# Kernel optimization log

Measured on AMD Instinct MI355X. Metric: run time of the kernel, lower is better.

The kernel has to match this reference:

```python
import jax, jax.numpy as jnp
import numpy as np

N_NODES = 20000
HEADS = 4


def _gat_conv(x, src, dst, W, att_src, att_dst, bias, concat):
    # PyG GATConv: h = x @ W -> [N, H, C]; edge score = leaky_relu(a_s[src]+a_d[dst], 0.2);
    # segment softmax over dst; scatter-add weighted messages.
    N = x.shape[0]
    H, C = att_src.shape[1], att_src.shape[2]
    h = (x @ W).reshape(N, H, C)
    a_s = jnp.sum(h * att_src, axis=-1)  # [N, H]
    a_d = jnp.sum(h * att_dst, axis=-1)  # [N, H]
    e = jax.nn.leaky_relu(a_s[src] + a_d[dst], negative_slope=0.2)  # [E, H]
    m = jax.ops.segment_max(e, dst, num_segments=N)  # [N, H]
    e = jnp.exp(e - m[dst])
    denom = jax.ops.segment_sum(e, dst, num_segments=N)
    alpha = e / (denom[dst] + 1e-16)  # [E, H]
    msg = h[src] * alpha[:, :, None]  # [E, H, C]
    out = jax.ops.segment_sum(msg, dst, num_segments=N)  # [N, H, C]
    if concat:
        out = out.reshape(N, H * C)
    else:
        out = out.mean(axis=1)
    return out + bias


def setup_inputs() -> dict:
    key = jax.random.key(0)
    ks = jax.random.split(key, 16)
    N, F_in, Hd, H, Z = N_NODES, 256, 128, HEADS, 64
    E = 320000
    x = jax.random.normal(ks[0], (N, F_in), dtype=jnp.float32)
    edge_index = jax.random.randint(ks[1], (2, E), 0, N, dtype=jnp.int64)
    def xavier(k, shape):
        fan_in, fan_out = shape[0], shape[1]
        lim = float(np.sqrt(6.0 / (fan_in + fan_out)))
        return jax.random.uniform(k, shape, jnp.float32, -lim, lim)
    inp = {"x": x, "edge_index": edge_index}
    dims = [(F_in, Hd), (Hd * H, Hd), (Hd * H, Hd)]
    for i, (din, dout) in enumerate(dims, 1):
        inp[f"W{i}"] = xavier(ks[2 * i], (din, H * dout))
        inp[f"att{i}_src"] = jax.random.normal(ks[2 * i + 1], (1, H, dout), dtype=jnp.float32) * 0.1
        inp[f"att{i}_dst"] = jax.random.normal(jax.random.fold_in(ks[2 * i + 1], 7), (1, H, dout), dtype=jnp.float32) * 0.1
        bdim = H * dout if i < 3 else dout
        inp[f"b{i}"] = jnp.zeros((bdim,), dtype=jnp.float32)
    inp["fc_W"] = xavier(ks[10], (Hd, 2 * Z))
    inp["fc_b"] = jnp.zeros((2 * Z,), dtype=jnp.float32)
    return inp


def reference(x, edge_index, W1, att1_src, att1_dst, b1, W2, att2_src, att2_dst, b2,
              W3, att3_src, att3_dst, b3, fc_W, fc_b):
    N = x.shape[0]
    # add_self_loops=True (PyG default)
    loop = jnp.arange(N, dtype=edge_index.dtype)
    src = jnp.concatenate([edge_index[0], loop])
    dst = jnp.concatenate([edge_index[1], loop])
    h = jax.nn.leaky_relu(_gat_conv(x, src, dst, W1, att1_src, att1_dst, b1, True), 0.01)
    h = jax.nn.leaky_relu(_gat_conv(h, src, dst, W2, att2_src, att2_dst, b2, True), 0.01)
    h = _gat_conv(h, src, dst, W3, att3_src, att3_dst, b3, False)
    z = h @ fc_W + fc_b
    mu, logvar = jnp.split(z, 2, axis=1)
    return (mu, jnp.exp(logvar))
```

## Files before the change

kernel.cpp:

```cpp
#include <hip/hip_runtime.h>
#include <hip/hip_bf16.h>

typedef unsigned short u16;
typedef unsigned int u32;
typedef __attribute__((ext_vector_type(8))) short bf16x8;
typedef __attribute__((ext_vector_type(4))) float f32x4;
typedef __attribute__((ext_vector_type(8))) u16 u16x8;
typedef __attribute__((ext_vector_type(4))) u16 u16x4;

#define NN 20000
#define NE 320000
#define HC 512

__device__ __forceinline__ float bf2f(u16 u){ return __uint_as_float(((u32)u)<<16); }
__device__ __forceinline__ u16 f2bf(float x){
  __hip_bfloat16 h = __float2bfloat16(x);
  return *reinterpret_cast<u16*>(&h);
}
__device__ __forceinline__ float escore(float x){
  float e = x > 0.f ? x : 0.2f*x;
  return __expf(fminf(e, 80.f));
}

__global__ __launch_bounds__(256) void cast_kernel(const float* __restrict__ in, u16* __restrict__ out, int total){
  int i = (blockIdx.x*256 + threadIdx.x)*4;
  if (i >= total) return;
  float4 v = *(const float4*)(in + i);
  u16x4 o = { f2bf(v.x), f2bf(v.y), f2bf(v.z), f2bf(v.w) };
  *(u16x4*)(out + i) = o;
}

__global__ __launch_bounds__(256) void transpose_cast(const float* __restrict__ W, u16* __restrict__ WT,
                                                      int K, int N){
  __shared__ u16 t[32][33];
  int bx = blockIdx.x*32;
  int by = blockIdx.y*32;
  int tx = threadIdx.x & 31, ty = threadIdx.x >> 5;
  for (int r = ty; r < 32; r += 8) t[r][tx] = f2bf(W[(size_t)(by+r)*N + bx + tx]);
  __syncthreads();
  for (int r = ty; r < 32; r += 8) WT[(size_t)(bx+r)*K + by + tx] = t[tx][r];
}

__global__ void detect_kernel(const int* __restrict__ ei, int* __restrict__ flag){
  __shared__ int nz;
  if (threadIdx.x == 0) nz = 0;
  __syncthreads();
  int c = 0;
  for (int k = threadIdx.x; k < 4096; k += 256) if (ei[2*k + 1] != 0) c++;
  atomicAdd(&nz, c);
  __syncthreads();
  if (threadIdx.x == 0) *flag = (nz == 0) ? 1 : 0;
}

__global__ __launch_bounds__(256) void normalize_edges(const int* __restrict__ ei, const int* __restrict__ flag,
    int* __restrict__ src, int* __restrict__ dst, int E){
  int e = blockIdx.x*256 + threadIdx.x;
  if (e >= E) return;
  if (*flag){ src[e] = ei[2*e]; dst[e] = ei[2*(E + e)]; }
  else      { src[e] = ei[e];   dst[e] = ei[E + e]; }
}

__global__ __launch_bounds__(256) void gemm_bf16(const u16* __restrict__ A, const u16* __restrict__ BT,
                                                 u16* __restrict__ C, int M, int K){
  __shared__ __align__(16) u16 Ads[128][64];
  __shared__ __align__(16) u16 Bds[128][64];
  const int bm = blockIdx.x, bn = blockIdx.y;
  const int tid = threadIdx.x;
  const int lane = tid & 63, wid = tid >> 6;
  const int wr = (wid >> 1) << 6, wc = (wid & 1) << 6;
  f32x4 acc[4][4] = {};
  const int row0 = bm*128;
  for (int k0 = 0; k0 < K; k0 += 64){
    #pragma unroll
    for (int p = 0; p < 4; ++p){
      int idx = p*256 + tid;
      int r = idx >> 3;
      int c = (idx & 7) << 3;
      int cs = c ^ ((r & 7) << 3);
      u16x8 va = {};
      int gr = row0 + r;
      if (gr < M) va = *(const u16x8*)(A + (size_t)gr*K + k0 + c);
      *(u16x8*)&Ads[r][cs] = va;
      u16x8 vb = *(const u16x8*)(BT + (size_t)(bn*128 + r)*K + k0 + c);
      *(u16x8*)&Bds[r][cs] = vb;
    }
    __syncthreads();
    #pragma unroll
    for (int kk = 0; kk < 64; kk += 32){
      const int lr = lane & 15;
      const int lk = kk + ((lane >> 4) << 3);
      bf16x8 a[4], b[4];
      #pragma unroll
      for (int i = 0; i < 4; ++i){
        int ar = wr + 16*i + lr;
        a[i] = *(const bf16x8*)&Ads[ar][lk ^ ((ar & 7) << 3)];
      }
      #pragma unroll
      for (int j = 0; j < 4; ++j){
        int br = wc + 16*j + lr;
        b[j] = *(const bf16x8*)&Bds[br][lk ^ ((br & 7) << 3)];
      }
      #pragma unroll
      for (int i = 0; i < 4; ++i)
        #pragma unroll
        for (int j = 0; j < 4; ++j)
          acc[i][j] = __builtin_amdgcn_mfma_f32_16x16x32_bf16(a[i], b[j], acc[i][j], 0, 0, 0);
    }
    __syncthreads();
  }
  const int lr = lane & 15, r4 = (lane >> 4) << 2;
  #pragma unroll
  for (int i = 0; i < 4; ++i)
    #pragma unroll
    for (int j = 0; j < 4; ++j){
      int col = bn*128 + wc + 16*j + lr;
      #pragma unroll
      for (int r = 0; r < 4; ++r){
        int row = row0 + wr + 16*i + r4 + r;
        if (row < M) C[(size_t)row*HC + col] = f2bf(acc[i][j][r]);
      }
    }
}

__global__ __launch_bounds__(256) void asad_kernel(const u16* __restrict__ h,
    const float* __restrict__ attS, const float* __restrict__ attD,
    float* __restrict__ a_s, float* __restrict__ a_d, int N){
  int wid = blockIdx.x*4 + (threadIdx.x >> 6);
  if (wid >= N) return;
  int lane = threadIdx.x & 63;
  u16x8 v = *(const u16x8*)(h + (size_t)wid*HC + lane*8);
  float4 s0 = *(const float4*)(attS + lane*8);
  float4 s1 = *(const float4*)(attS + lane*8 + 4);
  float4 d0 = *(const float4*)(attD + lane*8);
  float4 d1 = *(const float4*)(attD + lane*8 + 4);
  float sv[8] = {s0.x,s0.y,s0.z,s0.w,s1.x,s1.y,s1.z,s1.w};
  float dv[8] = {d0.x,d0.y,d0.z,d0.w,d1.x,d1.y,d1.z,d1.w};
  float ps = 0.f, pd = 0.f;
  #pragma unroll
  for (int t = 0; t < 8; ++t){ float hv = bf2f(v[t]); ps += hv*sv[t]; pd += hv*dv[t]; }
  #pragma unroll
  for (int off = 1; off < 16; off <<= 1){
    ps += __shfl_xor(ps, off, 64);
    pd += __shfl_xor(pd, off, 64);
  }
  if ((lane & 15) == 0){
    int hh = lane >> 4;
    a_s[wid*4 + hh] = ps;
    a_d[wid*4 + hh] = pd;
  }
}

__global__ __launch_bounds__(256) void hist_kernel(const int* __restrict__ dst, int* __restrict__ cnt, int E){
  int e = blockIdx.x*256 + threadIdx.x;
  if (e < E) atomicAdd(&cnt[dst[e]], 1);
}

__global__ __launch_bounds__(1024) void scan_kernel(const int* __restrict__ cnt,
    int* __restrict__ offs, int* __restrict__ cur, int N){
  __shared__ int bsum[1024];
  int tid = threadIdx.x;
  const int CH = (N + 1023) >> 10;
  int lo = tid*CH, hi = min(lo + CH, N);
  int s = 0;
  for (int i = lo; i < hi; ++i) s += cnt[i];
  bsum[tid] = s;
  __syncthreads();
  for (int off = 1; off < 1024; off <<= 1){
    int t = (tid >= off) ? bsum[tid - off] : 0;
    __syncthreads();
    bsum[tid] += t;
    __syncthreads();
  }
  int run = (tid > 0) ? bsum[tid - 1] : 0;
  for (int i = lo; i < hi; ++i){
    offs[i] = run; cur[i] = run; run += cnt[i];
  }
  if (tid == 1023) offs[N] = bsum[1023];
}

__global__ __launch_bounds__(256) void scatter_kernel(const int* __restrict__ src, const int* __restrict__ dst,
    int* __restrict__ cur, int* __restrict__ src_sorted, int E){
  int e = blockIdx.x*256 + threadIdx.x;
  if (e >= E) return;
  int d = dst[e];
  int pos = atomicAdd(&cur[d], 1);
  src_sorted[pos] = src[e];
}

template<int MODE>
__global__ __launch_bounds__(256) void agg_kernel(const u16* __restrict__ h,
    const int* __restrict__ srcs, const int* __restrict__ offs,
    const float* __restrict__ a_s, const float* __restrict__ a_d,
    const float* __restrict__ bias, void* __restrict__ outp, int N){
  int d = blockIdx.x*4 + (threadIdx.x >> 6);
  if (d >= N) return;
  int lane = threadIdx.x & 63;
  int head = lane >> 4;
  float adv = a_d[d*4 + head];
  float acc[8];
  float dsum;
  {
    float w = escore(a_s[d*4 + head] + adv);
    dsum = w;
    u16x8 v = *(const u16x8*)(h + (size_t)d*HC + lane*8);
    #pragma unroll
    for (int t = 0; t < 8; ++t) acc[t] = w*bf2f(v[t]);
  }
  int p0 = offs[d], p1 = offs[d+1];
  int p = p0;
  for (; p + 3 < p1; p += 4){
    int s0 = srcs[p], s1 = srcs[p+1], s2 = srcs[p+2], s3 = srcs[p+3];
    float w0 = escore(a_s[s0*4 + head] + adv);
    float w1 = escore(a_s[s1*4 + head] + adv);
    float w2 = escore(a_s[s2*4 + head] + adv);
    float w3 = escore(a_s[s3*4 + head] + adv);
    u16x8 v0 = *(const u16x8*)(h + (size_t)s0*HC + lane*8);
    u16x8 v1 = *(const u16x8*)(h + (size_t)s1*HC + lane*8);
    u16x8 v2 = *(const u16x8*)(h + (size_t)s2*HC + lane*8);
    u16x8 v3 = *(const u16x8*)(h + (size_t)s3*HC + lane*8);
    dsum += w0 + w1 + w2 + w3;
    #pragma unroll
    for (int t = 0; t < 8; ++t)
      acc[t] += w0*bf2f(v0[t]) + w1*bf2f(v1[t]) + w2*bf2f(v2[t]) + w3*bf2f(v3[t]);
  }
  for (; p < p1; ++p){
    int s = srcs[p];
    float w = escore(a_s[s*4 + head] + adv);
    u16x8 v = *(const u16x8*)(h + (size_t)s*HC + lane*8);
    dsum += w;
    #pragma unroll
    for (int t = 0; t < 8; ++t) acc[t] += w*bf2f(v[t]);
  }
  float inv = 1.0f / (dsum + 1e-16f);
  if (MODE < 2){
    u16* act = (u16*)outp;
    u16x8 o;
    #pragma unroll
    for (int t = 0; t < 8; ++t){
      float x = acc[t]*inv + bias[lane*8 + t];
      x = x > 0.f ? x : 0.01f*x;
      o[t] = f2bf(x);
    }
    *(u16x8*)(act + (size_t)d*HC + lane*8) = o;
  } else {
    #pragma unroll
    for (int t = 0; t < 8; ++t){
      acc[t] *= inv;
      acc[t] += __shfl_xor(acc[t], 16, 64);
      acc[t] += __shfl_xor(acc[t], 32, 64);
    }
    if (lane < 16){
      float* hf = (float*)outp;
      int c0 = lane*8;
      float4 o0 = {0.25f*acc[0] + bias[c0+0], 0.25f*acc[1] + bias[c0+1],
                   0.25f*acc[2] + bias[c0+2], 0.25f*acc[3] + bias[c0+3]};
      float4 o1 = {0.25f*acc[4] + bias[c0+4], 0.25f*acc[5] + bias[c0+5],
                   0.25f*acc[6] + bias[c0+6], 0.25f*acc[7] + bias[c0+7]};
      *(float4*)(hf + (size_t)d*128 + c0)     = o0;
      *(float4*)(hf + (size_t)d*128 + c0 + 4) = o1;
    }
  }
}

__global__ __launch_bounds__(128) void fc_kernel(const float* __restrict__ hfin, const float* __restrict__ W,
    const float* __restrict__ b, float* __restrict__ outp, int N){
  __shared__ float hl[128];
  int n = blockIdx.x, o = threadIdx.x;
  hl[o] = hfin[(size_t)n*128 + o];
  __syncthreads();
  float acc = b[o];
  #pragma unroll 8
  for (int k = 0; k < 128; ++k) acc += hl[k]*W[k*128 + o];
  if (o < 64) outp[(size_t)n*64 + o] = acc;
  else        outp[(size_t)N*64 + (size_t)n*64 + (o - 64)] = expf(acc);
}

extern "C" void kernel_launch(void* const* d_in, const int* in_sizes, int n_in,
                              void* d_out, int out_size, void* d_ws, size_t ws_size,
                              hipStream_t stream){
  const float* x    = (const float*)d_in[0];
  const int* ei     = (const int*)d_in[1];
  const float* W1   = (const float*)d_in[2];
  const float* att1s= (const float*)d_in[3];
  const float* att1d= (const float*)d_in[4];
  const float* b1   = (const float*)d_in[5];
  const float* W2   = (const float*)d_in[6];
  const float* att2s= (const float*)d_in[7];
  const float* att2d= (const float*)d_in[8];
  const float* b2   = (const float*)d_in[9];
  const float* W3   = (const float*)d_in[10];
  const float* att3s= (const float*)d_in[11];
  const float* att3d= (const float*)d_in[12];
  const float* b3   = (const float*)d_in[13];
  const float* fcW  = (const float*)d_in[14];
  const float* fcb  = (const float*)d_in[15];
  float* outp = (float*)d_out;

  char* ws = (char*)d_ws;
  size_t off = 0;
  auto alloc = [&](size_t bytes) -> void* {
    void* p = ws + off;
    off = (off + bytes + 255) & ~(size_t)255;
    return p;
  };
  u16*   xb     = (u16*)  alloc((size_t)NN*256*2);
  u16*   h      = (u16*)  alloc((size_t)NN*HC*2);
  u16*   act    = (u16*)  alloc((size_t)NN*HC*2);
  float* hfin   = (float*)alloc((size_t)NN*128*4);
  float* a_s    = (float*)alloc((size_t)NN*4*4);
  float* a_d    = (float*)alloc((size_t)NN*4*4);
  int*   cnt    = (int*)  alloc((size_t)NN*4);
  int*   cur    = (int*)  alloc((size_t)NN*4);
  int*   offs   = (int*)  alloc((size_t)(NN+1)*4);
  int*   src32  = (int*)  alloc((size_t)NE*4);
  int*   dst32  = (int*)  alloc((size_t)NE*4);
  int*   srcs   = (int*)  alloc((size_t)NE*4);
  u16*   WT1    = (u16*)  alloc((size_t)512*256*2);
  u16*   WT2    = (u16*)  alloc((size_t)512*512*2);
  u16*   WT3    = (u16*)  alloc((size_t)512*512*2);
  int*   flag   = (int*)  alloc(256);

  cast_kernel<<<5000, 256, 0, stream>>>(x, xb, NN*256);
  transpose_cast<<<dim3(16, 8),  256, 0, stream>>>(W1, WT1, 256, 512);
  transpose_cast<<<dim3(16, 16), 256, 0, stream>>>(W2, WT2, 512, 512);
  transpose_cast<<<dim3(16, 16), 256, 0, stream>>>(W3, WT3, 512, 512);

  detect_kernel<<<1, 256, 0, stream>>>(ei, flag);
  normalize_edges<<<1250, 256, 0, stream>>>(ei, flag, src32, dst32, NE);

  hipMemsetAsync(cnt, 0, (size_t)NN*4, stream);
  hist_kernel<<<1250, 256, 0, stream>>>(dst32, cnt, NE);
  scan_kernel<<<1, 1024, 0, stream>>>(cnt, offs, cur, NN);
  scatter_kernel<<<1250, 256, 0, stream>>>(src32, dst32, cur, srcs, NE);

  const float* attS[3] = {att1s, att2s, att3s};
  const float* attD[3] = {att1d, att2d, att3d};
  const u16*   WT[3]   = {WT1, WT2, WT3};
  const int    Kd[3]   = {256, 512, 512};

  for (int layer = 0; layer < 3; ++layer){
    const u16* Ain = (layer == 0) ? xb : act;
    gemm_bf16<<<dim3(157, 4), 256, 0, stream>>>(Ain, WT[layer], h, NN, Kd[layer]);
    asad_kernel<<<5000, 256, 0, stream>>>(h, attS[layer], attD[layer], a_s, a_d, NN);
    if (layer == 0)
      agg_kernel<0><<<5000, 256, 0, stream>>>(h, srcs, offs, a_s, a_d, b1, act, NN);
    else if (layer == 1)
      agg_kernel<1><<<5000, 256, 0, stream>>>(h, srcs, offs, a_s, a_d, b2, act, NN);
    else
      agg_kernel<2><<<5000, 256, 0, stream>>>(h, srcs, offs, a_s, a_d, b3, hfin, NN);
  }

  fc_kernel<<<NN, 128, 0, stream>>>(hfin, fcW, fcb, outp, NN);
}
```

Before: 351.2 us.

## Precompute attention alphas, split aggregation per half-row, use LDS-direct GEMM loads, fuse head-mean into FC

The GEMM tile loads now use global_load_lds to copy directly into shared memory with swizzled source addressing, replacing the register round trip. A new alpha_kernel computes normalized softmax weights per edge and per self loop once per layer. The aggregation kernel then reads those weights instead of recomputing exponentials, and it runs two waves per node, each covering half of the channels, to raise parallelism. The layer-3 head mean and bias are moved into a persistent FC kernel that keeps W in LDS, at the cost of an extra edge-sized alpha buffer written and read per layer.

```diff
diff --git a/kernel.cpp b/kernel.cpp
--- a/kernel.cpp
+++ b/kernel.cpp
@@ -20,6 +20,12 @@
 __device__ __forceinline__ float escore(float x){
   float e = x > 0.f ? x : 0.2f*x;
   return __expf(fminf(e, 80.f));
+}
+
+typedef const __attribute__((address_space(1))) unsigned int* gas_t;
+typedef __attribute__((address_space(3))) unsigned int* las_t;
+__device__ __forceinline__ void gl16(const void* g, void* l){
+  __builtin_amdgcn_global_load_lds((gas_t)g, (las_t)l, 16, 0, 0);
 }
 
 __global__ __launch_bounds__(256) void cast_kernel(const float* __restrict__ in, u16* __restrict__ out, int total){
@@ -70,19 +76,16 @@
   const int wr = (wid >> 1) << 6, wc = (wid & 1) << 6;
   f32x4 acc[4][4] = {};
   const int row0 = bm*128;
+  const int wbase = tid & 192;
   for (int k0 = 0; k0 < K; k0 += 64){
     #pragma unroll
     for (int p = 0; p < 4; ++p){
       int idx = p*256 + tid;
-      int r = idx >> 3;
-      int c = (idx & 7) << 3;
-      int cs = c ^ ((r & 7) << 3);
-      u16x8 va = {};
-      int gr = row0 + r;
-      if (gr < M) va = *(const u16x8*)(A + (size_t)gr*K + k0 + c);
-      *(u16x8*)&Ads[r][cs] = va;
-      u16x8 vb = *(const u16x8*)(BT + (size_t)(bn*128 + r)*K + k0 + c);
-      *(u16x8*)&Bds[r][cs] = vb;
+      int r = idx >> 3, cg = idx & 7;
+      int csg = cg ^ (r & 7);
+      int gr = row0 + r; if (gr >= M) gr = M - 1;
+      gl16(A + (size_t)gr*K + k0 + csg*8, (u16*)Ads + (size_t)(p*256 + wbase)*8);
+      gl16(BT + (size_t)(bn*128 + r)*K + k0 + csg*8, (u16*)Bds + (size_t)(p*256 + wbase)*8);
     }
     __syncthreads();
     #pragma unroll
@@ -187,92 +190,126 @@
   src_sorted[pos] = src[e];
 }
 
+__global__ __launch_bounds__(256) void alpha_kernel(const int* __restrict__ srcs, const int* __restrict__ offs,
+    const float* __restrict__ a_s, const float* __restrict__ a_d,
+    float* __restrict__ alpha, float* __restrict__ aself, int N){
+  int d = blockIdx.x*4 + (threadIdx.x >> 6);
+  if (d >= N) return;
+  int lane = threadIdx.x & 63;
+  int hh = lane & 3;
+  float adv = a_d[d*4 + hh];
+  float eself = escore(a_s[d*4 + hh] + adv);
+  int p0 = offs[d], p1 = offs[d+1];
+  float esum = 0.f;
+  for (int base = p0; base < p1; base += 16){
+    int el = base + (lane >> 2);
+    if (el < p1){
+      int s = srcs[el];
+      esum += escore(a_s[s*4 + hh] + adv);
+    }
+  }
+  esum += __shfl_xor(esum, 4, 64);
+  esum += __shfl_xor(esum, 8, 64);
+  esum += __shfl_xor(esum, 16, 64);
+  esum += __shfl_xor(esum, 32, 64);
+  float inv = 1.f/(esum + eself + 1e-16f);
+  if (lane < 4) aself[d*4 + hh] = eself*inv;
+  for (int base = p0; base < p1; base += 16){
+    int el = base + (lane >> 2);
+    if (el < p1){
+      int s = srcs[el];
+      alpha[(size_t)el*4 + hh] = escore(a_s[s*4 + hh] + adv)*inv;
+    }
+  }
+}
+
 template<int MODE>
 __global__ __launch_bounds__(256) void agg_kernel(const u16* __restrict__ h,
     const int* __restrict__ srcs, const int* __restrict__ offs,
-    const float* __restrict__ a_s, const float* __restrict__ a_d,
-    const float* __restrict__ bias, void* __restrict__ outp, int N){
-  int d = blockIdx.x*4 + (threadIdx.x >> 6);
+    const float* __restrict__ alpha, const float* __restrict__ aself,
+    const float* __restrict__ bias, u16* __restrict__ outp, int N){
+  int item = blockIdx.x*4 + (threadIdx.x >> 6);
+  int d = item >> 1, half = item & 1;
   if (d >= N) return;
   int lane = threadIdx.x & 63;
-  int head = lane >> 4;
-  float adv = a_d[d*4 + head];
-  float acc[8];
-  float dsum;
+  int c0 = half*256 + lane*4;
+  int head = c0 >> 7;
+  const u16* hb = h + c0;
+  float acc0, acc1, acc2, acc3;
   {
-    float w = escore(a_s[d*4 + head] + adv);
-    dsum = w;
-    u16x8 v = *(const u16x8*)(h + (size_t)d*HC + lane*8);
-    #pragma unroll
-    for (int t = 0; t < 8; ++t) acc[t] = w*bf2f(v[t]);
+    float w = aself[d*4 + head];
+    u16x4 v = *(const u16x4*)(hb + (size_t)d*HC);
+    acc0 = w*bf2f(v[0]); acc1 = w*bf2f(v[1]); acc2 = w*bf2f(v[2]); acc3 = w*bf2f(v[3]);
   }
   int p0 = offs[d], p1 = offs[d+1];
   int p = p0;
   for (; p + 3 < p1; p += 4){
     int s0 = srcs[p], s1 = srcs[p+1], s2 = srcs[p+2], s3 = srcs[p+3];
-    float w0 = escore(a_s[s0*4 + head] + adv);
-    float w1 = escore(a_s[s1*4 + head] + adv);
-    float w2 = escore(a_s[s2*4 + head] + adv);
-    float w3 = escore(a_s[s3*4 + head] + adv);
-    u16x8 v0 = *(const u16x8*)(h + (size_t)s0*HC + lane*8);
-    u16x8 v1 = *(const u16x8*)(h + (size_t)s1*HC + lane*8);
-    u16x8 v2 = *(const u16x8*)(h + (size_t)s2*HC + lane*8);
-    u16x8 v3 = *(const u16x8*)(h + (size_t)s3*HC + lane*8);
-    dsum += w0 + w1 + w2 + w3;
-    #pragma unroll
-    for (int t = 0; t < 8; ++t)
-      acc[t] += w0*bf2f(v0[t]) + w1*bf2f(v1[t]) + w2*bf2f(v2[t]) + w3*bf2f(v3[t]);
+    float w0 = alpha[(size_t)p*4 + head];
+    float w1 = alpha[(size_t)(p+1)*4 + head];
+    float w2 = alpha[(size_t)(p+2)*4 + head];
+    float w3 = alpha[(size_t)(p+3)*4 + head];
+    u16x4 v0 = *(const u16x4*)(hb + (size_t)s0*HC);
+    u16x4 v1 = *(const u16x4*)(hb + (size_t)s1*HC);
+    u16x4 v2 = *(const u16x4*)(hb + (size_t)s2*HC);
+    u16x4 v3 = *(const u16x4*)(hb + (size_t)s3*HC);
+    acc0 += w0*bf2f(v0[0]) + w1*bf2f(v1[0]) + w2*bf2f(v2[0]) + w3*bf2f(v3[0]);
+    acc1 += w0*bf2f(v0[1]) + w1*bf2f(v1[1]) + w2*bf2f(v2[1]) + w3*bf2f(v3[1]);
+    acc2 += w0*bf2f(v0[2]) + w1*bf2f(v1[2]) + w2*bf2f(v2[2]) + w3*bf2f(v3[2]);
+    acc3 += w0*bf2f(v0[3]) + w1*bf2f(v1[3]) + w2*bf2f(v2[3]) + w3*bf2f(v3[3]);
   }
   for (; p < p1; ++p){
     int s = srcs[p];
-    float w = escore(a_s[s*4 + head] + adv);
-    u16x8 v = *(const u16x8*)(h + (size_t)s*HC + lane*8);
-    dsum += w;
-    #pragma unroll
-    for (int t = 0; t < 8; ++t) acc[t] += w*bf2f(v[t]);
-  }
-  float inv = 1.0f / (dsum + 1e-16f);
-  if (MODE < 2){
-    u16* act = (u16*)outp;
-    u16x8 o;
-    #pragma unroll
-    for (int t = 0; t < 8; ++t){
-      float x = acc[t]*inv + bias[lane*8 + t];
-      x = x > 0.f ? x : 0.01f*x;
-      o[t] = f2bf(x);
-    }
-    *(u16x8*)(act + (size_t)d*HC + lane*8) = o;
+    float w = alpha[(size_t)p*4 + head];
+    u16x4 v = *(const u16x4*)(hb + (size_t)s*HC);
+    acc0 += w*bf2f(v[0]); acc1 += w*bf2f(v[1]); acc2 += w*bf2f(v[2]); acc3 += w*bf2f(v[3]);
+  }
+  if (MODE == 0){
+    float4 b = *(const float4*)(bias + c0);
+    float x0 = acc0 + b.x; x0 = x0 > 0.f ? x0 : 0.01f*x0;
+    float x1 = acc1 + b.y; x1 = x1 > 0.f ? x1 : 0.01f*x1;
+    float x2 = acc2 + b.z; x2 = x2 > 0.f ? x2 : 0.01f*x2;
+    float x3 = acc3 + b.w; x3 = x3 > 0.f ? x3 : 0.01f*x3;
+    u16x4 o = { f2bf(x0), f2bf(x1), f2bf(x2), f2bf(x3) };
+    *(u16x4*)(outp + (size_t)d*HC + c0) = o;
   } else {
-    #pragma unroll
-    for (int t = 0; t < 8; ++t){
-      acc[t] *= inv;
-      acc[t] += __shfl_xor(acc[t], 16, 64);
-      acc[t] += __shfl_xor(acc[t], 32, 64);
-    }
-    if (lane < 16){
-      float* hf = (float*)outp;
-      int c0 = lane*8;
-      float4 o0 = {0.25f*acc[0] + bias[c0+0], 0.25f*acc[1] + bias[c0+1],
-                   0.25f*acc[2] + bias[c0+2], 0.25f*acc[3] + bias[c0+3]};
-      float4 o1 = {0.25f*acc[4] + bias[c0+4], 0.25f*acc[5] + bias[c0+5],
-                   0.25f*acc[6] + bias[c0+6], 0.25f*acc[7] + bias[c0+7]};
-      *(float4*)(hf + (size_t)d*128 + c0)     = o0;
-      *(float4*)(hf + (size_t)d*128 + c0 + 4) = o1;
-    }
-  }
-}
-
-__global__ __launch_bounds__(128) void fc_kernel(const float* __restrict__ hfin, const float* __restrict__ W,
-    const float* __restrict__ b, float* __restrict__ outp, int N){
-  __shared__ float hl[128];
-  int n = blockIdx.x, o = threadIdx.x;
-  hl[o] = hfin[(size_t)n*128 + o];
-  __syncthreads();
-  float acc = b[o];
-  #pragma unroll 8
-  for (int k = 0; k < 128; ++k) acc += hl[k]*W[k*128 + o];
-  if (o < 64) outp[(size_t)n*64 + o] = acc;
-  else        outp[(size_t)N*64 + (size_t)n*64 + (o - 64)] = expf(acc);
+    u16x4 o = { f2bf(0.25f*acc0), f2bf(0.25f*acc1), f2bf(0.25f*acc2), f2bf(0.25f*acc3) };
+    *(u16x4*)(outp + (size_t)d*HC + c0) = o;
+  }
+}
+
+__global__ __launch_bounds__(256) void fc_kernel2(const u16* __restrict__ tmp, const float* __restrict__ b3,
+    const float* __restrict__ W, const float* __restrict__ fcb, float* __restrict__ outp,
+    int N, int nblocks){
+  __shared__ float Wl[128*128];
+  __shared__ float hsl[4][128];
+  int tid = threadIdx.x;
+  for (int i = tid*4; i < 16384; i += 1024)
+    *(float4*)&Wl[i] = *(const float4*)(W + i);
+  __syncthreads();
+  int w = tid >> 6, lane = tid & 63;
+  float2 bc = *(const float2*)(fcb + 2*lane);
+  float b3a = b3[lane], b3b = b3[64 + lane];
+  for (int n = blockIdx.x*4 + w; n < N; n += nblocks*4){
+    const u16* tp = tmp + (size_t)n*HC;
+    float h0 = (bf2f(tp[lane])      + bf2f(tp[128+lane]) + bf2f(tp[256+lane]) + bf2f(tp[384+lane])) + b3a;
+    float h1 = (bf2f(tp[64+lane])   + bf2f(tp[192+lane]) + bf2f(tp[320+lane]) + bf2f(tp[448+lane])) + b3b;
+    hsl[w][lane] = h0; hsl[w][64 + lane] = h1;
+    float acc0 = bc.x, acc1 = bc.y;
+    #pragma unroll 4
+    for (int k = 0; k < 128; ++k){
+      float hk = hsl[w][k];
+      float2 wv = *(const float2*)&Wl[k*128 + 2*lane];
+      acc0 += hk*wv.x; acc1 += hk*wv.y;
+    }
+    if (lane < 32){
+      float2 o = { acc0, acc1 };
+      *(float2*)(outp + (size_t)n*64 + 2*lane) = o;
+    } else {
+      float2 o = { expf(acc0), expf(acc1) };
+      *(float2*)(outp + (size_t)N*64 + (size_t)n*64 + (2*lane - 64)) = o;
+    }
+  }
 }
 
 extern "C" void kernel_launch(void* const* d_in, const int* in_sizes, int n_in,
@@ -306,9 +343,10 @@
   u16*   xb     = (u16*)  alloc((size_t)NN*256*2);
   u16*   h      = (u16*)  alloc((size_t)NN*HC*2);
   u16*   act    = (u16*)  alloc((size_t)NN*HC*2);
-  float* hfin   = (float*)alloc((size_t)NN*128*4);
   float* a_s    = (float*)alloc((size_t)NN*4*4);
   float* a_d    = (float*)alloc((size_t)NN*4*4);
+  float* aself  = (float*)alloc((size_t)NN*4*4);
+  float* alpha  = (float*)alloc((size_t)NE*4*4);
   int*   cnt    = (int*)  alloc((size_t)NN*4);
   int*   cur    = (int*)  alloc((size_t)NN*4);
   int*   offs   = (int*)  alloc((size_t)(NN+1)*4);
@@ -342,13 +380,14 @@
     const u16* Ain = (layer == 0) ? xb : act;
     gemm_bf16<<<dim3(157, 4), 256, 0, stream>>>(Ain, WT[layer], h, NN, Kd[layer]);
     asad_kernel<<<5000, 256, 0, stream>>>(h, attS[layer], attD[layer], a_s, a_d, NN);
+    alpha_kernel<<<5000, 256, 0, stream>>>(srcs, offs, a_s, a_d, alpha, aself, NN);
     if (layer == 0)
-      agg_kernel<0><<<5000, 256, 0, stream>>>(h, srcs, offs, a_s, a_d, b1, act, NN);
+      agg_kernel<0><<<10000, 256, 0, stream>>>(h, srcs, offs, alpha, aself, b1, act, NN);
     else if (layer == 1)
-      agg_kernel<1><<<5000, 256, 0, stream>>>(h, srcs, offs, a_s, a_d, b2, act, NN);
+      agg_kernel<0><<<10000, 256, 0, stream>>>(h, srcs, offs, alpha, aself, b2, act, NN);
     else
-      agg_kernel<2><<<5000, 256, 0, stream>>>(h, srcs, offs, a_s, a_d, b3, hfin, NN);
-  }
-
-  fc_kernel<<<NN, 128, 0, stream>>>(hfin, fcW, fcb, outp, NN);
-}
+      agg_kernel<1><<<10000, 256, 0, stream>>>(h, srcs, offs, alpha, aself, b3, act, NN);
+  }
+
+  fc_kernel2<<<256, 256, 0, stream>>>(act, b3, fcW, fcb, outp, NN, 256);
+}
```

Result: slower. 388.8 us (+10.7%).
